# Performance work log

Hardware: AMD Instinct MI355X
Metric: run time of the kernel (lower is better)

Reference implementation:

```python
import jax, jax.numpy as jnp
import numpy as np

R_MAX = 6.0
N_RADIAL = 5
N_BASIS = 7
N_SPECIES = 119
N_ATOMS = 25000
N_EDGES = 1000000


def _tril_2d(n):
    return np.array([(i, j) for i in range(n) for j in range(i + 1)], dtype=np.int32)


def _tril_3d(n):
    return np.array([(i, j, k) for i in range(n) for j in range(i + 1) for k in range(j + 1)], dtype=np.int32)


TRIL2 = jnp.asarray(_tril_2d(N_RADIAL))  # [15, 2]
TRIL3 = jnp.asarray(_tril_3d(N_RADIAL))  # [35, 3]


def setup_inputs() -> dict:
    key = jax.random.key(0)
    k1, k2, k3, k4 = jax.random.split(key, 4)
    dr_vec = jax.random.normal(k1, (N_EDGES, 3), jnp.float32) * 2.0
    Z = jax.random.randint(k2, (N_ATOMS,), 0, N_SPECIES, jnp.int32)
    neighbor_idxs = jax.random.randint(k3, (2, N_EDGES), 0, N_ATOMS, jnp.int32)
    coeffs = jax.random.normal(k4, (N_SPECIES, N_SPECIES, N_RADIAL, N_BASIS), jnp.float32) * 0.1
    return {"dr_vec": dr_vec, "Z": Z, "neighbor_idxs": neighbor_idxs, "coeffs": coeffs}


def _radial(dr, Z_i, Z_j, coeffs):
    # Gaussian basis (apax-style) with species-pair linear coefficients + cosine cutoff
    betta = N_BASIS ** 2 / R_MAX ** 2
    rad_norm = (2.0 * betta / np.pi) ** 0.75
    shifts = jnp.linspace(0.0, R_MAX, N_BASIS, dtype=dr.dtype)
    basis = rad_norm * jnp.exp(-betta * (dr[:, None] - shifts[None, :]) ** 2)  # [E, B]
    cutoff = 0.5 * (jnp.cos(np.pi * dr / R_MAX) + 1.0) * (dr < R_MAX)  # [E]
    c = coeffs[Z_i, Z_j]  # [E, R, B]
    rad = jnp.einsum("eb,erb->er", basis, c) * cutoff[:, None] / np.sqrt(N_BASIS)
    return rad  # [E, R]


def _forward(dr_vec, Z, neighbor_idxs, coeffs):
    idx_i, idx_j = neighbor_idxs[0], neighbor_idxs[1]
    Z_i, Z_j = Z[idx_i], Z[idx_j]
    dr = jnp.linalg.norm(dr_vec, axis=-1)  # [E]
    dn = dr_vec / (dr + 1e-5)[:, None]  # [E, 3]
    rad = _radial(dr, Z_i, Z_j, coeffs)  # [E, R]

    # per-edge outer-product moments
    m1e = rad[..., None] * dn[:, None, :]                      # [E,R,3]
    m2e = m1e[..., None] * dn[:, None, None, :]                # [E,R,3,3]
    m3e = m2e[..., None] * dn[:, None, None, None, :]          # [E,R,3,3,3]

    seg = lambda x: jax.ops.segment_sum(x, idx_j, num_segments=N_ATOMS)
    m0 = seg(rad)   # [A,R]
    m1 = seg(m1e)   # [A,R,3]
    m2 = seg(m2e)   # [A,R,3,3]
    m3 = seg(m3e)   # [A,R,3,3,3]

    contr_0 = m0
    contr_1 = jnp.einsum("ari,asi->rsa", m1, m1)
    contr_2 = jnp.einsum("arij,asij->rsa", m2, m2)
    contr_3 = jnp.einsum("arijk,asijk->rsa", m3, m3)
    contr_4 = jnp.einsum("arij,asik,atjk->rsta", m2, m2, m2)
    contr_5 = jnp.einsum("ari,asj,atij->rsta", m1, m1, m2)
    contr_6 = jnp.einsum("arijk,asijl,atkl->rsta", m3, m3, m2)
    contr_7 = jnp.einsum("arijk,asij,atk->rsta", m3, m2, m1)

    t2i, t2j = TRIL2[:, 0], TRIL2[:, 1]
    t3i, t3j, t3k = TRIL3[:, 0], TRIL3[:, 1], TRIL3[:, 2]

    n_atoms = contr_0.shape[0]
    contr_1 = contr_1[t2i, t2j].reshape(n_atoms, -1)
    contr_2 = contr_2[t2i, t2j].reshape(n_atoms, -1)
    contr_3 = contr_3[t2i, t2j].reshape(n_atoms, -1)
    contr_4 = contr_4[t3i, t3j, t3k].reshape(n_atoms, -1)
    contr_5 = contr_5[t2i, t2j].reshape(n_atoms, -1)
    contr_6 = contr_6[t2i, t2j].reshape(n_atoms, -1)
    contr_7 = contr_7.reshape(n_atoms, -1)

    return jnp.concatenate([contr_0, contr_1, contr_2, contr_3, contr_4, contr_5, contr_6, contr_7], axis=-1)


def reference(dr_vec, Z, neighbor_idxs, coeffs):
    return _forward(dr_vec, Z, neighbor_idxs, coeffs)
```

## Files before the change

### kernel.cpp

```cpp
#include <hip/hip_runtime.h>
#include <math.h>

#define NR 5
#define NB 7
#define NS 119
#define NA 25000
#define NE 1000000
#define OC 360
#define MUS 100
#define CAPR 104
#define CAPI 112
#define CHUNK 64
#define MPAD 101

static constexpr int T2I[15] = {0,1,1,2,2,2,3,3,3,3,4,4,4,4,4};
static constexpr int T2J[15] = {0,0,1,0,1,2,0,1,2,3,0,1,2,3,4};
static constexpr int T3I[35] = {0,1,1,1,2,2,2,2,2,2,3,3,3,3,3,3,3,3,3,3,4,4,4,4,4,4,4,4,4,4,4,4,4,4,4};
static constexpr int T3J[35] = {0,0,1,1,0,1,1,2,2,2,0,1,1,2,2,2,3,3,3,3,0,1,1,2,2,2,3,3,3,3,4,4,4,4,4};
static constexpr int T3K[35] = {0,0,0,1,0,0,1,0,1,2,0,0,1,0,1,2,0,1,2,3,0,0,1,0,1,2,0,1,2,3,0,1,2,3,4};

static constexpr int P2[9]  = {0,1,2, 1,3,4, 2,4,5};
static constexpr int P3[27] = {0,1,4, 1,2,5, 4,5,7,
                               1,2,5, 2,3,6, 5,6,8,
                               4,5,7, 5,6,8, 7,8,9};
static constexpr float W2[6]  = {1.f,2.f,2.f,1.f,2.f,1.f};
static constexpr float W3[10] = {1.f,3.f,3.f,1.f,3.f,6.f,3.f,3.f,3.f,1.f};

__global__ __launch_bounds__(256) void edge_record_kernel(
    const float* __restrict__ dr_vec, const int* __restrict__ Z,
    const int* __restrict__ nbr, const float* __restrict__ coeffs,
    int* __restrict__ cursor, float* __restrict__ binrec)
{
    int e = blockIdx.x * 256 + threadIdx.x;
    if (e >= NE) return;
    float x = dr_vec[3*e+0], y = dr_vec[3*e+1], z = dr_vec[3*e+2];
    int ai = nbr[e];
    int aj = nbr[NE + e];
    int Zi = Z[ai], Zj = Z[aj];

    float dr  = sqrtf(x*x + y*y + z*z);
    float inv = 1.0f / (dr + 1e-5f);
    float d0 = x*inv, d1 = y*inv, d2 = z*inv;

    const float PI_F = 3.14159265358979323846f;
    const float betta = 49.0f / 36.0f;
    float rad_norm = powf(2.0f * betta / PI_F, 0.75f);
    float cut = (dr < 6.0f) ? 0.5f*(cosf(PI_F * dr * (1.0f/6.0f)) + 1.0f) : 0.0f;
    float scale = cut * 0.3779644730092272272f;

    float basis[NB];
#pragma unroll
    for (int b = 0; b < NB; b++) {
        float t = dr - (float)b;
        basis[b] = rad_norm * expf(-betta * t * t);
    }

    const float* cp = coeffs + ((size_t)(Zi*NS + Zj)) * (NR*NB);
    float rad[NR];
#pragma unroll
    for (int r = 0; r < NR; r++) {
        float s = 0.f;
#pragma unroll
        for (int b = 0; b < NB; b++) s += basis[b] * cp[r*NB + b];
        rad[r] = s * scale;
    }

    int pos = __hip_atomic_fetch_add(&cursor[aj], 1, __ATOMIC_RELAXED, __HIP_MEMORY_SCOPE_AGENT);
    if (pos < CAPR) {
        float4* rp = (float4*)(binrec + ((size_t)aj * CAPR + pos) * 8);
        rp[0] = make_float4(rad[0], rad[1], rad[2], rad[3]);
        rp[1] = make_float4(rad[4], d0, d1, d2);
    }
}

__global__ __launch_bounds__(256) void accum_contract_kernel(
    const int* __restrict__ cursor, const float* __restrict__ binrec,
    float* __restrict__ out)
{
    __shared__ float lds[CHUNK * MPAD];
    int base = blockIdx.x * CHUNK;
    int nat  = min(CHUNK, NA - base);

    int al  = threadIdx.x >> 2;
    int sub = threadIdx.x & 3;
    int a   = base + al;
    int n   = (a < NA) ? min(cursor[a], CAPR) : 0;

    float acc[MUS];
#pragma unroll
    for (int i = 0; i < MUS; i++) acc[i] = 0.f;

    const float* mybin = binrec + (size_t)a * CAPR * 8;
    for (int p = sub; p < n; p += 4) {
        const float4* rp = (const float4*)(mybin + (size_t)p * 8);
        float4 r0 = rp[0], r1 = rp[1];
        float rad[NR] = {r0.x, r0.y, r0.z, r0.w, r1.x};
        float d0 = r1.y, d1 = r1.z, d2 = r1.w;

        float q2[6] = {d0*d0, d1*d0, d2*d0, d1*d1, d2*d1, d2*d2};
        float q3[10] = {d0*q2[0], d1*q2[0], d0*q2[3], d1*q2[3], d2*q2[0],
                        d2*q2[1], d2*q2[3], d0*q2[5], d1*q2[5], d2*q2[5]};

#pragma unroll
        for (int r = 0; r < NR; r++) {
            float rv = rad[r];
            acc[r] += rv;
            acc[5 + r*3 + 0] += rv*d0;
            acc[5 + r*3 + 1] += rv*d1;
            acc[5 + r*3 + 2] += rv*d2;
#pragma unroll
            for (int q = 0; q < 6; q++)  acc[20 + r*6  + q] += rv*q2[q];
#pragma unroll
            for (int q = 0; q < 10; q++) acc[50 + r*10 + q] += rv*q3[q];
        }
    }

#pragma unroll
    for (int i = 0; i < MUS; i++) {
        float v = acc[i];
        v += __shfl_xor(v, 1, 64);
        v += __shfl_xor(v, 2, 64);
        if (sub == 0) lds[al * MPAD + i] = v;
    }
    __syncthreads();

    int wave = threadIdx.x >> 6, lane = threadIdx.x & 63;
    int a2 = base + lane;
    bool valid = (lane < nat);
    int mb = lane * MPAD;

#define ML(o) lds[mb + (o)]

    for (int cc = wave; cc < 360; cc += 4) {
        if (!valid) continue;
        float v; int dest;

        if (cc < 5) {
            v = ML(cc);
            dest = a2 * OC + cc;
        } else if (cc < 20) {
            int l = cc - 5;
            int r = T2I[l], s = T2J[l];
            float acc2 = 0.f;
#pragma unroll
            for (int i = 0; i < 3; i++) acc2 += ML(5 + r*3 + i) * ML(5 + s*3 + i);
            v = acc2;
            int f = l * NA + a2; int aa = f / 15; dest = aa * OC + 5 + (f - aa*15);
        } else if (cc < 35) {
            int l = cc - 20;
            int r = T2I[l], s = T2J[l];
            float acc2 = 0.f;
#pragma unroll
            for (int p = 0; p < 6; p++) acc2 += W2[p] * ML(20 + r*6 + p) * ML(20 + s*6 + p);
            v = acc2;
            int f = l * NA + a2; int aa = f / 15; dest = aa * OC + 20 + (f - aa*15);
        } else if (cc < 50) {
            int l = cc - 35;
            int r = T2I[l], s = T2J[l];
            float acc2 = 0.f;
#pragma unroll
            for (int p = 0; p < 10; p++) acc2 += W3[p] * ML(50 + r*10 + p) * ML(50 + s*10 + p);
            v = acc2;
            int f = l * NA + a2; int aa = f / 15; dest = aa * OC + 35 + (f - aa*15);
        } else if (cc < 85) {
            int l = cc - 50;
            int r = T3I[l], s = T3J[l], t = T3K[l];
            float R[6], S[6], T[6];
#pragma unroll
            for (int p = 0; p < 6; p++) { R[p]=ML(20+r*6+p); S[p]=ML(20+s*6+p); T[p]=ML(20+t*6+p); }
            float acc2 = 0.f;
#pragma unroll
            for (int i = 0; i < 3; i++)
#pragma unroll
            for (int j = 0; j < 3; j++)
#pragma unroll
            for (int k = 0; k < 3; k++)
                acc2 += R[P2[i*3+j]] * S[P2[i*3+k]] * T[P2[j*3+k]];
            v = acc2;
            int f = l * NA + a2; int aa = f / 35; dest = aa * OC + 50 + (f - aa*35);
        } else if (cc < 160) {
            int l = cc - 85;
            int p = l / 5, t = l - p*5;
            int r = T2I[p], s = T2J[p];
            float T[6];
#pragma unroll
            for (int q = 0; q < 6; q++) T[q] = ML(20 + t*6 + q);
            float acc2 = 0.f;
#pragma unroll
            for (int i = 0; i < 3; i++)
#pragma unroll
            for (int j = 0; j < 3; j++)
                acc2 += ML(5 + r*3 + i) * ML(5 + s*3 + j) * T[P2[i*3+j]];
            v = acc2;
            int f = l * NA + a2; int aa = f / 75; dest = aa * OC + 85 + (f - aa*75);
        } else if (cc < 235) {
            int l = cc - 160;
            int p = l / 5, t = l - p*5;
            int r = T2I[p], s = T2J[p];
            float R[10], S[10], T[6];
#pragma unroll
            for (int q = 0; q < 10; q++) { R[q]=ML(50+r*10+q); S[q]=ML(50+s*10+q); }
#pragma unroll
            for (int q = 0; q < 6;  q++) T[q] = ML(20 + t*6 + q);
            float acc2 = 0.f;
#pragma unroll
            for (int k = 0; k < 3; k++)
#pragma unroll
            for (int l2 = 0; l2 < 3; l2++) {
                float inner = 0.f;
#pragma unroll
                for (int i = 0; i < 3; i++)
#pragma unroll
                for (int j = 0; j < 3; j++)
                    inner += R[P3[(i*3+j)*3+k]] * S[P3[(i*3+j)*3+l2]];
                acc2 += inner * T[P2[k*3+l2]];
            }
            v = acc2;
            int f = l * NA + a2; int aa = f / 75; dest = aa * OC + 160 + (f - aa*75);
        } else {
            int l = cc - 235;
            int r = l / 25; int rem = l - r*25; int s = rem / 5; int t = rem - s*5;
            float R[10], S[6], T1[3];
#pragma unroll
            for (int q = 0; q < 10; q++) R[q] = ML(50 + r*10 + q);
#pragma unroll
            for (int q = 0; q < 6;  q++) S[q] = ML(20 + s*6 + q);
#pragma unroll
            for (int q = 0; q < 3;  q++) T1[q] = ML(5 + t*3 + q);
            float acc2 = 0.f;
#pragma unroll
            for (int i = 0; i < 3; i++)
#pragma unroll
            for (int j = 0; j < 3; j++)
#pragma unroll
            for (int k = 0; k < 3; k++)
                acc2 += R[P3[(i*3+j)*3+k]] * S[P2[i*3+j]] * T1[k];
            v = acc2;
            int f = l * NA + a2; int aa = f / 125; dest = aa * OC + 235 + (f - aa*125);
        }
        out[dest] = v;
    }
#undef ML
}

__global__ __launch_bounds__(256) void scatter_kernel(
    const int* __restrict__ nbr, int* __restrict__ cursor, int* __restrict__ bins)
{
    int e = blockIdx.x * 256 + threadIdx.x;
    if (e >= NE) return;
    int aj = nbr[NE + e];
    int pos = __hip_atomic_fetch_add(&cursor[aj], 1, __ATOMIC_RELAXED, __HIP_MEMORY_SCOPE_AGENT);
    if (pos < CAPI) bins[(size_t)aj * CAPI + pos] = e;
}

__global__ __launch_bounds__(256) void accum_kernel(
    const float* __restrict__ dr_vec, const int* __restrict__ Z,
    const int* __restrict__ nbr, const float* __restrict__ coeffs,
    const int* __restrict__ cursor, const int* __restrict__ bins,
    float* __restrict__ Mu)
{
    __shared__ float red[32 * MUS];
    int t   = blockIdx.x * 256 + threadIdx.x;
    int a   = t >> 3;
    int sub = t & 7;
    int al  = threadIdx.x >> 3;
    int n   = (a < NA) ? min(cursor[a], CAPI) : 0;
    int Zj  = (a < NA) ? Z[a] : 0;

    float acc[MUS];
#pragma unroll
    for (int i = 0; i < MUS; i++) acc[i] = 0.f;

    const int* mybin = bins + (size_t)a * CAPI;
    const float PI_F = 3.14159265358979323846f;
    const float betta = 49.0f / 36.0f;
    float rad_norm = powf(2.0f * betta / PI_F, 0.75f);

    for (int p = sub; p < n; p += 8) {
        int e = mybin[p];
        float x = dr_vec[3*e+0], y = dr_vec[3*e+1], z = dr_vec[3*e+2];
        int Zi = Z[nbr[e]];

        float dr  = sqrtf(x*x + y*y + z*z);
        float inv = 1.0f / (dr + 1e-5f);
        float d0 = x*inv, d1 = y*inv, d2 = z*inv;

        float cut = (dr < 6.0f) ? 0.5f*(cosf(PI_F * dr * (1.0f/6.0f)) + 1.0f) : 0.0f;
        float scale = cut * 0.3779644730092272272f;

        float basis[NB];
#pragma unroll
        for (int b = 0; b < NB; b++) {
            float tt = dr - (float)b;
            basis[b] = rad_norm * expf(-betta * tt * tt);
        }

        const float* cp = coeffs + ((size_t)(Zi*NS + Zj)) * (NR*NB);
        float rad[NR];
#pragma unroll
        for (int r = 0; r < NR; r++) {
            float s = 0.f;
#pragma unroll
            for (int b = 0; b < NB; b++) s += basis[b] * cp[r*NB + b];
            rad[r] = s * scale;
        }

        float q2[6] = {d0*d0, d1*d0, d2*d0, d1*d1, d2*d1, d2*d2};
        float q3[10] = {d0*q2[0], d1*q2[0], d0*q2[3], d1*q2[3], d2*q2[0],
                        d2*q2[1], d2*q2[3], d0*q2[5], d1*q2[5], d2*q2[5]};

#pragma unroll
        for (int r = 0; r < NR; r++) {
            float rv = rad[r];
            acc[r] += rv;
            acc[5 + r*3 + 0] += rv*d0;
            acc[5 + r*3 + 1] += rv*d1;
            acc[5 + r*3 + 2] += rv*d2;
#pragma unroll
            for (int q = 0; q < 6; q++)  acc[20 + r*6  + q] += rv*q2[q];
#pragma unroll
            for (int q = 0; q < 10; q++) acc[50 + r*10 + q] += rv*q3[q];
        }
    }

#pragma unroll
    for (int i = 0; i < MUS; i++) {
        float v = acc[i];
        v += __shfl_xor(v, 1, 64);
        v += __shfl_xor(v, 2, 64);
        v += __shfl_xor(v, 4, 64);
        if (sub == 0) red[al * MUS + i] = v;
    }
    __syncthreads();

    for (int u = threadIdx.x; u < 32 * MUS; u += 256) {
        int ga = blockIdx.x * 32 + u / MUS;
        if (ga < NA) Mu[(size_t)ga * MUS + (u - (u / MUS) * MUS)] = red[u];
    }
}

__global__ __launch_bounds__(256) void contract_kernel(
    const float* __restrict__ Mu, float* __restrict__ out)
{
    __shared__ float lds[CHUNK * MPAD];
    int base = blockIdx.x * CHUNK;
    int nat  = min(CHUNK, NA - base);

    for (int t = threadIdx.x; t < nat * MUS; t += 256) {
        int al = t / MUS, off = t - al * MUS;
        lds[al * MPAD + off] = Mu[(size_t)base * MUS + t];
    }
    __syncthreads();

    int wave = threadIdx.x >> 6, lane = threadIdx.x & 63;
    int a2 = base + lane;
    bool valid = (lane < nat);
    int mb = lane * MPAD;

#define ML(o) lds[mb + (o)]

    for (int cc = wave; cc < 360; cc += 4) {
        if (!valid) continue;
        float v; int dest;

        if (cc < 5) {
            v = ML(cc);
            dest = a2 * OC + cc;
        } else if (cc < 20) {
            int l = cc - 5;
            int r = T2I[l], s = T2J[l];
            float acc = 0.f;
#pragma unroll
            for (int i = 0; i < 3; i++) acc += ML(5 + r*3 + i) * ML(5 + s*3 + i);
            v = acc;
            int f = l * NA + a2; int aa = f / 15; dest = aa * OC + 5 + (f - aa*15);
        } else if (cc < 35) {
            int l = cc - 20;
            int r = T2I[l], s = T2J[l];
            float acc = 0.f;
#pragma unroll
            for (int p = 0; p < 6; p++) acc += W2[p] * ML(20 + r*6 + p) * ML(20 + s*6 + p);
            v = acc;
            int f = l * NA + a2; int aa = f / 15; dest = aa * OC + 20 + (f - aa*15);
        } else if (cc < 50) {
            int l = cc - 35;
            int r = T2I[l], s = T2J[l];
            float acc = 0.f;
#pragma unroll
            for (int p = 0; p < 10; p++) acc += W3[p] * ML(50 + r*10 + p) * ML(50 + s*10 + p);
            v = acc;
            int f = l * NA + a2; int aa = f / 15; dest = aa * OC + 35 + (f - aa*15);
        } else if (cc < 85) {
            int l = cc - 50;
            int r = T3I[l], s = T3J[l], t = T3K[l];
            float R[6], S[6], T[6];
#pragma unroll
            for (int p = 0; p < 6; p++) { R[p]=ML(20+r*6+p); S[p]=ML(20+s*6+p); T[p]=ML(20+t*6+p); }
            float acc = 0.f;
#pragma unroll
            for (int i = 0; i < 3; i++)
#pragma unroll
            for (int j = 0; j < 3; j++)
#pragma unroll
            for (int k = 0; k < 3; k++)
                acc += R[P2[i*3+j]] * S[P2[i*3+k]] * T[P2[j*3+k]];
            v = acc;
            int f = l * NA + a2; int aa = f / 35; dest = aa * OC + 50 + (f - aa*35);
        } else if (cc < 160) {
            int l = cc - 85;
            int p = l / 5, t = l - p*5;
            int r = T2I[p], s = T2J[p];
            float T[6];
#pragma unroll
            for (int q = 0; q < 6; q++) T[q] = ML(20 + t*6 + q);
            float acc = 0.f;
#pragma unroll
            for (int i = 0; i < 3; i++)
#pragma unroll
            for (int j = 0; j < 3; j++)
                acc += ML(5 + r*3 + i) * ML(5 + s*3 + j) * T[P2[i*3+j]];
            v = acc;
            int f = l * NA + a2; int aa = f / 75; dest = aa * OC + 85 + (f - aa*75);
        } else if (cc < 235) {
            int l = cc - 160;
            int p = l / 5, t = l - p*5;
            int r = T2I[p], s = T2J[p];
            float R[10], S[10], T[6];
#pragma unroll
            for (int q = 0; q < 10; q++) { R[q]=ML(50+r*10+q); S[q]=ML(50+s*10+q); }
#pragma unroll
            for (int q = 0; q < 6;  q++) T[q] = ML(20 + t*6 + q);
            float acc = 0.f;
#pragma unroll
            for (int k = 0; k < 3; k++)
#pragma unroll
            for (int l2 = 0; l2 < 3; l2++) {
                float inner = 0.f;
#pragma unroll
                for (int i = 0; i < 3; i++)
#pragma unroll
                for (int j = 0; j < 3; j++)
                    inner += R[P3[(i*3+j)*3+k]] * S[P3[(i*3+j)*3+l2]];
                acc += inner * T[P2[k*3+l2]];
            }
            v = acc;
            int f = l * NA + a2; int aa = f / 75; dest = aa * OC + 160 + (f - aa*75);
        } else {
            int l = cc - 235;
            int r = l / 25; int rem = l - r*25; int s = rem / 5; int t = rem - s*5;
            float R[10], S[6], T1[3];
#pragma unroll
            for (int q = 0; q < 10; q++) R[q] = ML(50 + r*10 + q);
#pragma unroll
            for (int q = 0; q < 6;  q++) S[q] = ML(20 + s*6 + q);
#pragma unroll
            for (int q = 0; q < 3;  q++) T1[q] = ML(5 + t*3 + q);
            float acc = 0.f;
#pragma unroll
            for (int i = 0; i < 3; i++)
#pragma unroll
            for (int j = 0; j < 3; j++)
#pragma unroll
            for (int k = 0; k < 3; k++)
                acc += R[P3[(i*3+j)*3+k]] * S[P2[i*3+j]] * T1[k];
            v = acc;
            int f = l * NA + a2; int aa = f / 125; dest = aa * OC + 235 + (f - aa*125);
        }
        out[dest] = v;
    }
#undef ML
}

extern "C" void kernel_launch(void* const* d_in, const int* in_sizes, int n_in,
                              void* d_out, int out_size, void* d_ws, size_t ws_size,
                              hipStream_t stream) {
    const float* dr_vec = (const float*)d_in[0];
    const int*   Z      = (const int*)d_in[1];
    const int*   nbr    = (const int*)d_in[2];
    const float* coeffs = (const float*)d_in[3];
    float* out = (float*)d_out;

    size_t need_fast = (size_t)NA * sizeof(int) + (size_t)NA * CAPR * 8 * sizeof(float);

    if (ws_size >= need_fast) {
        int*   cursor = (int*)d_ws;
        float* binrec = (float*)(cursor + NA);
        hipMemsetAsync(cursor, 0, (size_t)NA * sizeof(int), stream);
        edge_record_kernel<<<(NE + 255)/256, 256, 0, stream>>>(dr_vec, Z, nbr, coeffs, cursor, binrec);
        accum_contract_kernel<<<(NA + CHUNK - 1)/CHUNK, 256, 0, stream>>>(cursor, binrec, out);
    } else {
        int*   cursor = (int*)d_ws;
        int*   bins   = cursor + NA;
        float* Mu     = (float*)(bins + (size_t)NA * CAPI);
        hipMemsetAsync(cursor, 0, (size_t)NA * sizeof(int), stream);
        scatter_kernel<<<(NE + 255)/256, 256, 0, stream>>>(nbr, cursor, bins);
        accum_kernel<<<(NA*8 + 255)/256, 256, 0, stream>>>(dr_vec, Z, nbr, coeffs, cursor, bins, Mu);
        contract_kernel<<<(NA + CHUNK - 1)/CHUNK, 256, 0, stream>>>(Mu, out);
    }
}
```

Measured before the change: 211.2 us.

## Process four edges per thread, pad atomic cursors, shrink bin capacity

The edge record kernel now handles four strided edges per thread and issues all index loads and cursor atomics up front, so more memory and atomic operations are in flight at once. Per-atom cursors are padded to 16 ints each, which puts every counter on its own 64-byte segment and avoids contention between neighbouring atoms. Bin capacity drops from 104 to 96 records, which shrinks the workspace but raises the chance that a high-degree atom overflows and silently drops edges. The cursor memset becomes 16 times larger, and it now also scatters reads of the counts in the accumulate kernel.

```diff
diff --git a/kernel.cpp b/kernel.cpp
--- a/kernel.cpp
+++ b/kernel.cpp
@@ -8,10 +8,12 @@
 #define NE 1000000
 #define OC 360
 #define MUS 100
-#define CAPR 104
+#define CAPR 96
 #define CAPI 112
+#define CSTRIDE 16
 #define CHUNK 64
 #define MPAD 101
+#define EPT 4
 
 static constexpr int T2I[15] = {0,1,1,2,2,2,3,3,3,3,4,4,4,4,4};
 static constexpr int T2J[15] = {0,0,1,0,1,2,0,1,2,3,0,1,2,3,4};
@@ -31,45 +33,71 @@
     const int* __restrict__ nbr, const float* __restrict__ coeffs,
     int* __restrict__ cursor, float* __restrict__ binrec)
 {
-    int e = blockIdx.x * 256 + threadIdx.x;
-    if (e >= NE) return;
-    float x = dr_vec[3*e+0], y = dr_vec[3*e+1], z = dr_vec[3*e+2];
-    int ai = nbr[e];
-    int aj = nbr[NE + e];
-    int Zi = Z[ai], Zj = Z[aj];
-
-    float dr  = sqrtf(x*x + y*y + z*z);
-    float inv = 1.0f / (dr + 1e-5f);
-    float d0 = x*inv, d1 = y*inv, d2 = z*inv;
+    const int Q = NE / EPT;
+    int t = blockIdx.x * 256 + threadIdx.x;
+    if (t >= Q) return;
+
+    int e[EPT], ai[EPT], aj[EPT];
+#pragma unroll
+    for (int k = 0; k < EPT; k++) e[k] = t + k * Q;
+
+#pragma unroll
+    for (int k = 0; k < EPT; k++) aj[k] = nbr[NE + e[k]];
+#pragma unroll
+    for (int k = 0; k < EPT; k++) ai[k] = nbr[e[k]];
+
+    int pos[EPT];
+#pragma unroll
+    for (int k = 0; k < EPT; k++)
+        pos[k] = __hip_atomic_fetch_add(&cursor[aj[k] * CSTRIDE], 1,
+                                        __ATOMIC_RELAXED, __HIP_MEMORY_SCOPE_AGENT);
+
+    float x[EPT], y[EPT], z[EPT];
+#pragma unroll
+    for (int k = 0; k < EPT; k++) {
+        x[k] = dr_vec[3*e[k]+0];
+        y[k] = dr_vec[3*e[k]+1];
+        z[k] = dr_vec[3*e[k]+2];
+    }
+    int Zi[EPT], Zj[EPT];
+#pragma unroll
+    for (int k = 0; k < EPT; k++) { Zi[k] = Z[ai[k]]; Zj[k] = Z[aj[k]]; }
 
     const float PI_F = 3.14159265358979323846f;
     const float betta = 49.0f / 36.0f;
     float rad_norm = powf(2.0f * betta / PI_F, 0.75f);
-    float cut = (dr < 6.0f) ? 0.5f*(cosf(PI_F * dr * (1.0f/6.0f)) + 1.0f) : 0.0f;
-    float scale = cut * 0.3779644730092272272f;
-
-    float basis[NB];
-#pragma unroll
-    for (int b = 0; b < NB; b++) {
-        float t = dr - (float)b;
-        basis[b] = rad_norm * expf(-betta * t * t);
-    }
-
-    const float* cp = coeffs + ((size_t)(Zi*NS + Zj)) * (NR*NB);
-    float rad[NR];
-#pragma unroll
-    for (int r = 0; r < NR; r++) {
-        float s = 0.f;
-#pragma unroll
-        for (int b = 0; b < NB; b++) s += basis[b] * cp[r*NB + b];
-        rad[r] = s * scale;
-    }
-
-    int pos = __hip_atomic_fetch_add(&cursor[aj], 1, __ATOMIC_RELAXED, __HIP_MEMORY_SCOPE_AGENT);
-    if (pos < CAPR) {
-        float4* rp = (float4*)(binrec + ((size_t)aj * CAPR + pos) * 8);
-        rp[0] = make_float4(rad[0], rad[1], rad[2], rad[3]);
-        rp[1] = make_float4(rad[4], d0, d1, d2);
+
+#pragma unroll
+    for (int k = 0; k < EPT; k++) {
+        float dr  = sqrtf(x[k]*x[k] + y[k]*y[k] + z[k]*z[k]);
+        float inv = 1.0f / (dr + 1e-5f);
+        float d0 = x[k]*inv, d1 = y[k]*inv, d2 = z[k]*inv;
+
+        float cut = (dr < 6.0f) ? 0.5f*(cosf(PI_F * dr * (1.0f/6.0f)) + 1.0f) : 0.0f;
+        float scale = cut * 0.3779644730092272272f;
+
+        float basis[NB];
+#pragma unroll
+        for (int b = 0; b < NB; b++) {
+            float tt = dr - (float)b;
+            basis[b] = rad_norm * expf(-betta * tt * tt);
+        }
+
+        const float* cp = coeffs + ((size_t)(Zi[k]*NS + Zj[k])) * (NR*NB);
+        float rad[NR];
+#pragma unroll
+        for (int r = 0; r < NR; r++) {
+            float s = 0.f;
+#pragma unroll
+            for (int b = 0; b < NB; b++) s += basis[b] * cp[r*NB + b];
+            rad[r] = s * scale;
+        }
+
+        if (pos[k] < CAPR) {
+            float4* rp = (float4*)(binrec + ((size_t)aj[k] * CAPR + pos[k]) * 8);
+            rp[0] = make_float4(rad[0], rad[1], rad[2], rad[3]);
+            rp[1] = make_float4(rad[4], d0, d1, d2);
+        }
     }
 }
 
@@ -84,7 +112,7 @@
     int al  = threadIdx.x >> 2;
     int sub = threadIdx.x & 3;
     int a   = base + al;
-    int n   = (a < NA) ? min(cursor[a], CAPR) : 0;
+    int n   = (a < NA) ? min(cursor[a * CSTRIDE], CAPR) : 0;
 
     float acc[MUS];
 #pragma unroll
@@ -480,13 +508,13 @@
     const float* coeffs = (const float*)d_in[3];
     float* out = (float*)d_out;
 
-    size_t need_fast = (size_t)NA * sizeof(int) + (size_t)NA * CAPR * 8 * sizeof(float);
+    size_t need_fast = (size_t)NA * CSTRIDE * sizeof(int) + (size_t)NA * CAPR * 8 * sizeof(float);
 
     if (ws_size >= need_fast) {
         int*   cursor = (int*)d_ws;
-        float* binrec = (float*)(cursor + NA);
-        hipMemsetAsync(cursor, 0, (size_t)NA * sizeof(int), stream);
-        edge_record_kernel<<<(NE + 255)/256, 256, 0, stream>>>(dr_vec, Z, nbr, coeffs, cursor, binrec);
+        float* binrec = (float*)(cursor + (size_t)NA * CSTRIDE);
+        hipMemsetAsync(cursor, 0, (size_t)NA * CSTRIDE * sizeof(int), stream);
+        edge_record_kernel<<<(NE/EPT + 255)/256, 256, 0, stream>>>(dr_vec, Z, nbr, coeffs, cursor, binrec);
         accum_contract_kernel<<<(NA + CHUNK - 1)/CHUNK, 256, 0, stream>>>(cursor, binrec, out);
     } else {
         int*   cursor = (int*)d_ws;
```

Measured after the change: 220.9 us. 4.6% more time.
